# Optimization experiments

Measured on AMD Instinct MI355X. Metric: run time of the kernel, lower is better.

The kernel has to match this reference:

```python
import jax, jax.numpy as jnp
import numpy as np

NUM_HEADS = 16
NUM_KV_HEADS = 4
HEAD_DIM = 128
EPS = 1e-6


def _rotate_half(x):
    x1, x2 = jnp.split(x, 2, axis=-1)
    return jnp.concatenate((-x2, x1), axis=-1)


def _rms_norm(x, w):
    var = jnp.mean(x * x, axis=-1, keepdims=True)
    return x * jax.lax.rsqrt(var + EPS) * w


def setup_inputs() -> dict:
    key = jax.random.key(0)
    ks = jax.random.split(key, 6)
    B, S, H = 2, 2048, 2048
    hidden_states = jax.random.normal(ks[0], (B, S, H), dtype=jnp.float32)
    # real RoPE tables (HF-style: freqs tiled twice along last dim)
    inv_freq = 1.0 / (10000.0 ** (np.arange(0, HEAD_DIM, 2, dtype=np.float32) / HEAD_DIM))
    pos = np.arange(S, dtype=np.float32)
    ang = np.concatenate([pos[:, None] * inv_freq[None, :]] * 2, axis=-1)  # [S, head_dim]
    cos = jnp.broadcast_to(jnp.cos(ang)[None], (B, S, HEAD_DIM)).astype(jnp.float32)
    sin = jnp.broadcast_to(jnp.sin(ang)[None], (B, S, HEAD_DIM)).astype(jnp.float32)
    sc = 0.02
    Wq = jax.random.normal(ks[1], (NUM_HEADS * HEAD_DIM, H), dtype=jnp.float32) * sc
    Wk = jax.random.normal(ks[2], (NUM_KV_HEADS * HEAD_DIM, H), dtype=jnp.float32) * sc
    Wv = jax.random.normal(ks[3], (NUM_KV_HEADS * HEAD_DIM, H), dtype=jnp.float32) * sc
    Wo = jax.random.normal(ks[4], (H, NUM_HEADS * HEAD_DIM), dtype=jnp.float32) * sc
    q_norm_w = jnp.ones((HEAD_DIM,), dtype=jnp.float32)
    k_norm_w = jnp.ones((HEAD_DIM,), dtype=jnp.float32)
    return {"hidden_states": hidden_states, "cos": cos, "sin": sin,
            "Wq": Wq, "Wk": Wk, "Wv": Wv, "Wo": Wo,
            "q_norm_w": q_norm_w, "k_norm_w": k_norm_w}


def reference(hidden_states, cos, sin, Wq, Wk, Wv, Wo, q_norm_w, k_norm_w):
    B, S, H = hidden_states.shape
    groups = NUM_HEADS // NUM_KV_HEADS
    # projections (Linear: x @ W^T), then [B, h, S, d]
    q = (hidden_states @ Wq.T).reshape(B, S, NUM_HEADS, HEAD_DIM).transpose(0, 2, 1, 3)
    k = (hidden_states @ Wk.T).reshape(B, S, NUM_KV_HEADS, HEAD_DIM).transpose(0, 2, 1, 3)
    v = (hidden_states @ Wv.T).reshape(B, S, NUM_KV_HEADS, HEAD_DIM).transpose(0, 2, 1, 3)
    # per-head RMSNorm
    q = _rms_norm(q, q_norm_w)
    k = _rms_norm(k, k_norm_w)
    # RoPE, cos/sin broadcast over heads (unsqueeze_dim=1)
    c = cos[:, None, :, :]
    s = sin[:, None, :, :]
    q = q * c + _rotate_half(q) * s
    k = k * c + _rotate_half(k) * s
    # GQA: expand kv heads
    k = jnp.repeat(k, groups, axis=1)
    v = jnp.repeat(v, groups, axis=1)
    scale = 1.0 / jnp.sqrt(jnp.float32(HEAD_DIM))
    scores = jnp.einsum('bhqd,bhkd->bhqk', q, k) * scale
    attn = jax.nn.softmax(scores, axis=-1)
    out = jnp.einsum('bhqk,bhkd->bhqd', attn, v)
    out = out.transpose(0, 2, 1, 3).reshape(B, S, NUM_HEADS * HEAD_DIM)
    return out @ Wo.T
```

## Files before the change

### kernel.cpp

```cpp
#include <hip/hip_runtime.h>
#include <hip/hip_bf16.h>
#include <stdint.h>

typedef __attribute__((ext_vector_type(8))) short short8;
typedef __attribute__((ext_vector_type(4))) float floatx4;
typedef __attribute__((ext_vector_type(16))) float floatx16;

#define MFMA16(a, b, c) __builtin_amdgcn_mfma_f32_16x16x32_bf16(a, b, c, 0, 0, 0)
#define MFMA32(a, b, c) __builtin_amdgcn_mfma_f32_32x32x16_bf16(a, b, c, 0, 0, 0)

static __device__ __forceinline__ void gload_lds16(const __hip_bfloat16* g, __hip_bfloat16* l) {
  __builtin_amdgcn_global_load_lds(
      (const __attribute__((address_space(1))) void*)g,
      (__attribute__((address_space(3))) void*)l,
      16, 0, 0);
}

__global__ void f2bf(const float* __restrict__ in, __hip_bfloat16* __restrict__ out, int n) {
  const int stride = gridDim.x * blockDim.x * 4;
  for (int i = (blockIdx.x * blockDim.x + threadIdx.x) * 4; i < n; i += stride) {
    const float4 v = *(const float4*)(in + i);
    __hip_bfloat16 t[4] = {__float2bfloat16(v.x), __float2bfloat16(v.y),
                           __float2bfloat16(v.z), __float2bfloat16(v.w)};
    *(short4*)(out + i) = *(const short4*)t;
  }
}

template <typename OUT_T>
__global__ __launch_bounds__(256)
void gemm_bt(const __hip_bfloat16* __restrict__ A, const __hip_bfloat16* __restrict__ Bt,
             OUT_T* __restrict__ C, int M, int N, int K) {
  __shared__ __hip_bfloat16 As[2][128 * 32];
  __shared__ __hip_bfloat16 Bs[2][128 * 32];
  const int tid = threadIdx.x;
  const int wid = tid >> 6, lane = tid & 63;
  const int lg = lane >> 4, lr = lane & 15;
  const int wr = wid >> 1, wc = wid & 1;
  const int m0 = blockIdx.x * 128, n0 = blockIdx.y * 128;
  const int nk = K >> 5;

  floatx4 acc[4][4];
#pragma unroll
  for (int mi = 0; mi < 4; ++mi)
#pragma unroll
    for (int ni = 0; ni < 4; ++ni) acc[mi][ni] = (floatx4)(0.0f);

  auto stage = [&](int buf, int kt) {
    const int k0 = kt << 5;
#pragma unroll
    for (int i = 0; i < 2; ++i) {
      const int e = (i * 256 + tid) * 8;
      const int row = e >> 5, col = e & 31;
      gload_lds16(A + (size_t)(m0 + row) * K + k0 + col, &As[buf][e]);
    }
#pragma unroll
    for (int i = 0; i < 2; ++i) {
      const int e = (i * 256 + tid) * 8;
      const int row = e >> 5, col = e & 31;
      gload_lds16(Bt + (size_t)(n0 + row) * K + k0 + col, &Bs[buf][e]);
    }
  };

  stage(0, 0);
  __syncthreads();

  for (int kt = 0; kt < nk; ++kt) {
    const int cur = kt & 1;
    if (kt + 1 < nk) stage(cur ^ 1, kt + 1);
    short8 af[4], bfr[4];
#pragma unroll
    for (int mi = 0; mi < 4; ++mi)
      af[mi] = *(const short8*)&As[cur][(wr * 64 + mi * 16 + lr) * 32 + lg * 8];
#pragma unroll
    for (int ni = 0; ni < 4; ++ni)
      bfr[ni] = *(const short8*)&Bs[cur][(wc * 64 + ni * 16 + lr) * 32 + lg * 8];
#pragma unroll
    for (int mi = 0; mi < 4; ++mi)
#pragma unroll
      for (int ni = 0; ni < 4; ++ni) acc[mi][ni] = MFMA16(af[mi], bfr[ni], acc[mi][ni]);
    __syncthreads();
  }

#pragma unroll
  for (int mi = 0; mi < 4; ++mi)
#pragma unroll
    for (int ni = 0; ni < 4; ++ni) {
      const int row = m0 + wr * 64 + mi * 16 + lg * 4;
      const int col = n0 + wc * 64 + ni * 16 + lr;
#pragma unroll
      for (int r = 0; r < 4; ++r) {
        C[(size_t)(row + r) * N + col] = (OUT_T)acc[mi][ni][r];
      }
    }
}

__global__ __launch_bounds__(256)
void normrope(const __hip_bfloat16* __restrict__ qkv, const float* __restrict__ cosb,
              const float* __restrict__ sinb, const float* __restrict__ qw,
              const float* __restrict__ kw, __hip_bfloat16* __restrict__ Q,
              __hip_bfloat16* __restrict__ K, __hip_bfloat16* __restrict__ V) {
  const int m = blockIdx.x;
  const int b = m >> 11, s = m & 2047;
  const int wid = threadIdx.x >> 6, lane = threadIdx.x & 63;
  const size_t qkvrow = (size_t)m * 3072;
  const float c1 = cosb[(size_t)m * 128 + lane], s1 = sinb[(size_t)m * 128 + lane];
  const float c2 = cosb[(size_t)m * 128 + lane + 64], s2 = sinb[(size_t)m * 128 + lane + 64];
  for (int h = wid * 6; h < wid * 6 + 6; ++h) {
    const float x1 = __bfloat162float(qkv[qkvrow + h * 128 + lane]);
    const float x2 = __bfloat162float(qkv[qkvrow + h * 128 + lane + 64]);
    if (h < 20) {
      float ss = x1 * x1 + x2 * x2;
      ss += __shfl_xor(ss, 1);  ss += __shfl_xor(ss, 2);  ss += __shfl_xor(ss, 4);
      ss += __shfl_xor(ss, 8);  ss += __shfl_xor(ss, 16); ss += __shfl_xor(ss, 32);
      const float rs = rsqrtf(ss * (1.0f / 128.0f) + 1e-6f);
      const float* w = (h < 16) ? qw : kw;
      const float n1 = x1 * rs * w[lane], n2 = x2 * rs * w[lane + 64];
      const float o1 = n1 * c1 - n2 * s1;
      const float o2 = n2 * c2 + n1 * s2;
      if (h < 16) {
        const size_t base = ((size_t)(b * 16 + h) * 2048 + s) * 128;
        Q[base + lane] = __float2bfloat16(o1);
        Q[base + lane + 64] = __float2bfloat16(o2);
      } else {
        const size_t base = ((size_t)(b * 4 + h - 16) * 2048 + s) * 128;
        K[base + lane] = __float2bfloat16(o1);
        K[base + lane + 64] = __float2bfloat16(o2);
      }
    } else {
      const size_t base = ((size_t)(b * 4 + h - 20) * 2048 + s) * 128;
      V[base + lane] = qkv[qkvrow + h * 128 + lane];
      V[base + lane + 64] = qkv[qkvrow + h * 128 + lane + 64];
    }
  }
}

__global__ __launch_bounds__(256)
void vtrans(const __hip_bfloat16* __restrict__ V, __hip_bfloat16* __restrict__ Vt) {
  __shared__ short L[64 * 65];
  const int tid = threadIdx.x;
  const int s0 = blockIdx.x * 64, d0 = blockIdx.y * 64, bz = blockIdx.z;
  const __hip_bfloat16* src = V + (size_t)bz * 2048 * 128;
#pragma unroll
  for (int i = 0; i < 2; ++i) {
    const int slot = i * 256 + tid;
    const int srow = slot >> 3, c8 = (slot & 7) * 8;
    short8 v = *(const short8*)(src + (size_t)(s0 + srow) * 128 + d0 + c8);
#pragma unroll
    for (int j = 0; j < 8; ++j) L[(c8 + j) * 65 + srow] = v[j];
  }
  __syncthreads();
  __hip_bfloat16* dst = Vt + (size_t)bz * 128 * 2048;
#pragma unroll
  for (int i = 0; i < 2; ++i) {
    const int slot = i * 256 + tid;
    const int drow = slot >> 3, sc8 = (slot & 7) * 8;
    short8 o;
#pragma unroll
    for (int j = 0; j < 8; ++j) {
      const int p = sc8 + j;
      const int pb = p & 31;
      const int phys = (p & ~31) | ((pb & 3) + ((pb >> 2) & 1) * 8 + ((pb >> 3) & 1) * 4 + (pb & 16));
      o[j] = L[drow * 65 + phys];
    }
    *(short8*)(dst + (size_t)(d0 + drow) * 2048 + s0 + sc8) = o;
  }
}

__global__ __launch_bounds__(256, 2)
void fattn(const __hip_bfloat16* __restrict__ Qg, const __hip_bfloat16* __restrict__ Kg,
           const __hip_bfloat16* __restrict__ Vtg, __hip_bfloat16* __restrict__ Og) {
  __shared__ short SMEM[2][17920];

  const int tid = threadIdx.x, wid = tid >> 6, lane = tid & 63;
  const int l31 = lane & 31, hi = lane >> 5;
  const int qt = blockIdx.x, bh = blockIdx.y;
  const int b = bh >> 4, h = bh & 15, hkv = h >> 2;
  const int q0w = qt * 128 + wid * 32;

  const __hip_bfloat16* Qrow = Qg + ((size_t)((b * 16 + h) * 2048 + q0w + l31)) * 128;
  short8 qf2[8];
#pragma unroll
  for (int ks = 0; ks < 8; ++ks) qf2[ks] = *(const short8*)(Qrow + ks * 16 + hi * 8);

  const __hip_bfloat16* Kbase = Kg + (size_t)(b * 4 + hkv) * 2048 * 128;
  const __hip_bfloat16* Vtbase = Vtg + (size_t)(b * 4 + hkv) * 128 * 2048;

  int koff[4], kldsoff[4], voff[4], vldsoff[4];
#pragma unroll
  for (int i = 0; i < 4; ++i) {
    const int idx = i * 256 + tid;
    const int kkv = idx >> 4, kd = (idx & 15) * 8;
    koff[i] = kkv * 128 + kd;
    kldsoff[i] = kkv * 136 + kd;
    const int vd = idx >> 3, vc = (idx & 7) * 8;
    voff[i] = vd * 2048 + vc;
    vldsoff[i] = 8704 + vd * 72 + vc;
  }

  floatx16 oacc[4];
#pragma unroll
  for (int dblk = 0; dblk < 4; ++dblk) oacc[dblk] = (floatx16)(0.0f);
  floatx16 lacc = (floatx16)(0.0f);

  short8 ones;
#pragma unroll
  for (int j = 0; j < 8; ++j) ones[j] = (short)0x3F80;

  const float SC2 = 0.12753102497113446f;
  const float OFF2 = 17.31234049066756f;

  short8 kreg[4], vreg[4];
  auto loadKV = [&](int kt) {
    const __hip_bfloat16* kp = Kbase + (size_t)kt * 64 * 128;
    const __hip_bfloat16* vp = Vtbase + (size_t)kt * 64;
#pragma unroll
    for (int i = 0; i < 4; ++i) kreg[i] = *(const short8*)(kp + koff[i]);
#pragma unroll
    for (int i = 0; i < 4; ++i) vreg[i] = *(const short8*)(vp + voff[i]);
  };

  loadKV(0);
#pragma unroll
  for (int i = 0; i < 4; ++i) *(short8*)&SMEM[0][kldsoff[i]] = kreg[i];
#pragma unroll
  for (int i = 0; i < 4; ++i) *(short8*)&SMEM[0][vldsoff[i]] = vreg[i];
  loadKV(1);
  asm volatile("s_waitcnt lgkmcnt(0)" ::: "memory");
  __builtin_amdgcn_s_barrier();
  __builtin_amdgcn_sched_barrier(0);

  for (int kt = 0; kt < 32; ++kt) {
    const int cur = kt & 1;
    const short* Ksf = SMEM[cur];
    const short* Vtl = SMEM[cur];
    if (kt + 1 < 32) {
      short* nb = SMEM[cur ^ 1];
#pragma unroll
      for (int i = 0; i < 4; ++i) *(short8*)&nb[kldsoff[i]] = kreg[i];
#pragma unroll
      for (int i = 0; i < 4; ++i) *(short8*)&nb[vldsoff[i]] = vreg[i];
      if (kt + 2 < 32) loadKV(kt + 2);
    }

    floatx16 st[2];
    st[0] = (floatx16)(0.0f);
    st[1] = (floatx16)(0.0f);
    __builtin_amdgcn_s_setprio(1);
#pragma unroll
    for (int ks = 0; ks < 8; ++ks) {
      const short8 kf0 = *(const short8*)&Ksf[l31 * 136 + ks * 16 + hi * 8];
      const short8 kf1 = *(const short8*)&Ksf[(32 + l31) * 136 + ks * 16 + hi * 8];
      st[0] = MFMA32(kf0, qf2[ks], st[0]);
      st[1] = MFMA32(kf1, qf2[ks], st[1]);
    }
    __builtin_amdgcn_s_setprio(0);

    int pk[2][8];
#pragma unroll
    for (int kvblk = 0; kvblk < 2; ++kvblk)
#pragma unroll
      for (int m = 0; m < 8; ++m) {
        const float e0 = exp2f(fmaf(st[kvblk][2 * m], SC2, -OFF2));
        const float e1 = exp2f(fmaf(st[kvblk][2 * m + 1], SC2, -OFF2));
        asm("v_cvt_pk_bf16_f32 %0, %1, %2" : "=v"(pk[kvblk][m]) : "v"(e0), "v"(e1));
      }

#pragma unroll
    for (int kvblk = 0; kvblk < 2; ++kvblk) {
#pragma unroll
      for (int s = 0; s < 2; ++s) {
        union { int i[4]; short8 s8; } u;
        u.i[0] = pk[kvblk][4 * s + 0];
        u.i[1] = pk[kvblk][4 * s + 1];
        u.i[2] = pk[kvblk][4 * s + 2];
        u.i[3] = pk[kvblk][4 * s + 3];
        const short8 pB = u.s8;
        __builtin_amdgcn_s_setprio(1);
        lacc = MFMA32(ones, pB, lacc);
#pragma unroll
        for (int dblk = 0; dblk < 4; ++dblk) {
          const short8 vf =
              *(const short8*)&Vtl[8704 + (dblk * 32 + l31) * 72 + kvblk * 32 + s * 16 + hi * 8];
          oacc[dblk] = MFMA32(vf, pB, oacc[dblk]);
        }
        __builtin_amdgcn_s_setprio(0);
      }
    }

    asm volatile("s_waitcnt lgkmcnt(0)" ::: "memory");
    __builtin_amdgcn_s_barrier();
    __builtin_amdgcn_sched_barrier(0);
  }

  const float inv = 1.0f / lacc[0];
  short* tw = &SMEM[0][0] + wid * 4352;
#pragma unroll
  for (int dblk = 0; dblk < 4; ++dblk)
#pragma unroll
    for (int a = 0; a < 4; ++a) {
      __hip_bfloat16 o4[4];
#pragma unroll
      for (int r = 0; r < 4; ++r) o4[r] = __float2bfloat16(oacc[dblk][4 * a + r] * inv);
      *(short4*)&tw[l31 * 136 + dblk * 32 + a * 8 + hi * 4] = *(const short4*)o4;
    }
  __hip_bfloat16* orow =
      Og + ((size_t)(b * 2048 + q0w + (lane >> 1))) * 2048 + h * 128 + (lane & 1) * 64;
  const short* trow = &tw[(lane >> 1) * 136 + (lane & 1) * 64];
#pragma unroll
  for (int c = 0; c < 8; ++c) {
    *(short8*)(orow + c * 8) = *(const short8*)(trow + c * 8);
  }
}

extern "C" void kernel_launch(void* const* d_in, const int* in_sizes, int n_in,
                              void* d_out, int out_size, void* d_ws, size_t ws_size,
                              hipStream_t stream) {
  const float* hidden = (const float*)d_in[0];
  const float* cosb = (const float*)d_in[1];
  const float* sinb = (const float*)d_in[2];
  const float* Wq = (const float*)d_in[3];
  const float* Wk = (const float*)d_in[4];
  const float* Wv = (const float*)d_in[5];
  const float* Wo = (const float*)d_in[6];
  const float* qw = (const float*)d_in[7];
  const float* kw = (const float*)d_in[8];

  char* ws = (char*)d_ws;
  __hip_bfloat16* hidden_bf = (__hip_bfloat16*)ws; ws += (size_t)4096 * 2048 * 2;
  __hip_bfloat16* wqkv = (__hip_bfloat16*)ws;      ws += (size_t)3072 * 2048 * 2;
  __hip_bfloat16* wo_bf = (__hip_bfloat16*)ws;     ws += (size_t)2048 * 2048 * 2;
  __hip_bfloat16* qkv = (__hip_bfloat16*)ws;       ws += (size_t)4096 * 3072 * 2;
  __hip_bfloat16* Qb = (__hip_bfloat16*)ws;        ws += (size_t)2 * 16 * 2048 * 128 * 2;
  __hip_bfloat16* Kb = (__hip_bfloat16*)ws;        ws += (size_t)2 * 4 * 2048 * 128 * 2;
  __hip_bfloat16* Vb = (__hip_bfloat16*)ws;        ws += (size_t)2 * 4 * 2048 * 128 * 2;
  __hip_bfloat16* attn = (__hip_bfloat16*)ws;      ws += (size_t)4096 * 2048 * 2;
  __hip_bfloat16* Vt = wqkv;

  f2bf<<<1024, 256, 0, stream>>>(hidden, hidden_bf, 4096 * 2048);
  f2bf<<<1024, 256, 0, stream>>>(Wq, wqkv, 2048 * 2048);
  f2bf<<<512, 256, 0, stream>>>(Wk, wqkv + (size_t)2048 * 2048, 512 * 2048);
  f2bf<<<512, 256, 0, stream>>>(Wv, wqkv + (size_t)2560 * 2048, 512 * 2048);
  f2bf<<<1024, 256, 0, stream>>>(Wo, wo_bf, 2048 * 2048);

  gemm_bt<__hip_bfloat16><<<dim3(32, 24), 256, 0, stream>>>(hidden_bf, wqkv, qkv, 4096, 3072, 2048);
  normrope<<<4096, 256, 0, stream>>>(qkv, cosb, sinb, qw, kw, Qb, Kb, Vb);
  vtrans<<<dim3(32, 2, 8), 256, 0, stream>>>(Vb, Vt);
  fattn<<<dim3(16, 32), 256, 0, stream>>>(Qb, Kb, Vt, attn);
  gemm_bt<float><<<dim3(32, 16), 256, 0, stream>>>(attn, wo_bf, (float*)d_out, 4096, 2048, 2048);
}
```

Measured before the change: 243.5 us.

## Pre-block K/V tiles and stage them via direct global-to-LDS loads in attention

K and V are re-laid out into contiguous per-tile blocks by new kblock and vtrans2 kernels, with V transposed straight from the qkv buffer so the V copy in normrope goes away. The attention kernel then stages each K/V tile with global_load_lds instead of going through registers and LDS stores. The row sum is now accumulated in VALU from the exponentials instead of an extra MFMA against a ones vector. The intent is to cut register pressure and LDS store traffic in the attention loop, at the cost of an extra kernel pass over K and an unpadded LDS layout that may cause bank conflicts.

```diff
diff --git a/kernel.cpp b/kernel.cpp
--- a/kernel.cpp
+++ b/kernel.cpp
@@ -98,58 +98,68 @@
 void normrope(const __hip_bfloat16* __restrict__ qkv, const float* __restrict__ cosb,
               const float* __restrict__ sinb, const float* __restrict__ qw,
               const float* __restrict__ kw, __hip_bfloat16* __restrict__ Q,
-              __hip_bfloat16* __restrict__ K, __hip_bfloat16* __restrict__ V) {
+              __hip_bfloat16* __restrict__ K) {
   const int m = blockIdx.x;
   const int b = m >> 11, s = m & 2047;
   const int wid = threadIdx.x >> 6, lane = threadIdx.x & 63;
   const size_t qkvrow = (size_t)m * 3072;
   const float c1 = cosb[(size_t)m * 128 + lane], s1 = sinb[(size_t)m * 128 + lane];
   const float c2 = cosb[(size_t)m * 128 + lane + 64], s2 = sinb[(size_t)m * 128 + lane + 64];
-  for (int h = wid * 6; h < wid * 6 + 6; ++h) {
+  for (int h = wid * 5; h < wid * 5 + 5; ++h) {
     const float x1 = __bfloat162float(qkv[qkvrow + h * 128 + lane]);
     const float x2 = __bfloat162float(qkv[qkvrow + h * 128 + lane + 64]);
-    if (h < 20) {
-      float ss = x1 * x1 + x2 * x2;
-      ss += __shfl_xor(ss, 1);  ss += __shfl_xor(ss, 2);  ss += __shfl_xor(ss, 4);
-      ss += __shfl_xor(ss, 8);  ss += __shfl_xor(ss, 16); ss += __shfl_xor(ss, 32);
-      const float rs = rsqrtf(ss * (1.0f / 128.0f) + 1e-6f);
-      const float* w = (h < 16) ? qw : kw;
-      const float n1 = x1 * rs * w[lane], n2 = x2 * rs * w[lane + 64];
-      const float o1 = n1 * c1 - n2 * s1;
-      const float o2 = n2 * c2 + n1 * s2;
-      if (h < 16) {
-        const size_t base = ((size_t)(b * 16 + h) * 2048 + s) * 128;
-        Q[base + lane] = __float2bfloat16(o1);
-        Q[base + lane + 64] = __float2bfloat16(o2);
-      } else {
-        const size_t base = ((size_t)(b * 4 + h - 16) * 2048 + s) * 128;
-        K[base + lane] = __float2bfloat16(o1);
-        K[base + lane + 64] = __float2bfloat16(o2);
-      }
+    float ss = x1 * x1 + x2 * x2;
+    ss += __shfl_xor(ss, 1);  ss += __shfl_xor(ss, 2);  ss += __shfl_xor(ss, 4);
+    ss += __shfl_xor(ss, 8);  ss += __shfl_xor(ss, 16); ss += __shfl_xor(ss, 32);
+    const float rs = rsqrtf(ss * (1.0f / 128.0f) + 1e-6f);
+    const float* w = (h < 16) ? qw : kw;
+    const float n1 = x1 * rs * w[lane], n2 = x2 * rs * w[lane + 64];
+    const float o1 = n1 * c1 - n2 * s1;
+    const float o2 = n2 * c2 + n1 * s2;
+    if (h < 16) {
+      const size_t base = ((size_t)(b * 16 + h) * 2048 + s) * 128;
+      Q[base + lane] = __float2bfloat16(o1);
+      Q[base + lane + 64] = __float2bfloat16(o2);
     } else {
-      const size_t base = ((size_t)(b * 4 + h - 20) * 2048 + s) * 128;
-      V[base + lane] = qkv[qkvrow + h * 128 + lane];
-      V[base + lane + 64] = qkv[qkvrow + h * 128 + lane + 64];
+      const size_t base = ((size_t)(b * 4 + h - 16) * 2048 + s) * 128;
+      K[base + lane] = __float2bfloat16(o1);
+      K[base + lane + 64] = __float2bfloat16(o2);
     }
   }
 }
 
 __global__ __launch_bounds__(256)
-void vtrans(const __hip_bfloat16* __restrict__ V, __hip_bfloat16* __restrict__ Vt) {
+void kblock(const __hip_bfloat16* __restrict__ K, __hip_bfloat16* __restrict__ Kb2) {
+  const int z = blockIdx.y;
+  const int t = blockIdx.x * 4 + (threadIdx.x >> 6);
+  const int kv = threadIdx.x & 63;
+  const short* src = (const short*)K + (size_t)z * 262144 + t * 8192;
+  short* dst = (short*)Kb2 + (size_t)z * 262144 + t * 8192;
+#pragma unroll
+  for (int cd = 0; cd < 16; ++cd) {
+    const short8 v = *(const short8*)&src[kv * 128 + cd * 8];
+    *(short8*)&dst[cd * 512 + kv * 8] = v;
+  }
+}
+
+__global__ __launch_bounds__(256)
+void vtrans2(const __hip_bfloat16* __restrict__ qkv, __hip_bfloat16* __restrict__ Vt2) {
   __shared__ short L[64 * 65];
   const int tid = threadIdx.x;
-  const int s0 = blockIdx.x * 64, d0 = blockIdx.y * 64, bz = blockIdx.z;
-  const __hip_bfloat16* src = V + (size_t)bz * 2048 * 128;
+  const int t = blockIdx.x, d0 = blockIdx.y * 64, z = blockIdx.z;
+  const int b = z >> 2, hkv = z & 3;
+  const int s0 = t * 64;
 #pragma unroll
   for (int i = 0; i < 2; ++i) {
     const int slot = i * 256 + tid;
     const int srow = slot >> 3, c8 = (slot & 7) * 8;
-    short8 v = *(const short8*)(src + (size_t)(s0 + srow) * 128 + d0 + c8);
+    const short8 v = *(const short8*)((const short*)qkv +
+        (size_t)(b * 2048 + s0 + srow) * 3072 + 2560 + hkv * 128 + d0 + c8);
 #pragma unroll
     for (int j = 0; j < 8; ++j) L[(c8 + j) * 65 + srow] = v[j];
   }
   __syncthreads();
-  __hip_bfloat16* dst = Vt + (size_t)bz * 128 * 2048;
+  short* dst = (short*)Vt2 + (size_t)z * 262144 + t * 8192;
 #pragma unroll
   for (int i = 0; i < 2; ++i) {
     const int slot = i * 256 + tid;
@@ -162,19 +172,20 @@
       const int phys = (p & ~31) | ((pb & 3) + ((pb >> 2) & 1) * 8 + ((pb >> 3) & 1) * 4 + (pb & 16));
       o[j] = L[drow * 65 + phys];
     }
-    *(short8*)(dst + (size_t)(d0 + drow) * 2048 + s0 + sc8) = o;
+    *(short8*)&dst[(sc8 >> 3) * 1024 + (d0 + drow) * 8] = o;
   }
 }
 
 __global__ __launch_bounds__(256, 2)
-void fattn(const __hip_bfloat16* __restrict__ Qg, const __hip_bfloat16* __restrict__ Kg,
-           const __hip_bfloat16* __restrict__ Vtg, __hip_bfloat16* __restrict__ Og) {
-  __shared__ short SMEM[2][17920];
+void fattn(const __hip_bfloat16* __restrict__ Qg, const __hip_bfloat16* __restrict__ Kb2,
+           const __hip_bfloat16* __restrict__ Vt2, __hip_bfloat16* __restrict__ Og) {
+  __shared__ short SMEM[2][16384];
 
   const int tid = threadIdx.x, wid = tid >> 6, lane = tid & 63;
   const int l31 = lane & 31, hi = lane >> 5;
   const int qt = blockIdx.x, bh = blockIdx.y;
   const int b = bh >> 4, h = bh & 15, hkv = h >> 2;
+  const int z = b * 4 + hkv;
   const int q0w = qt * 128 + wid * 32;
 
   const __hip_bfloat16* Qrow = Qg + ((size_t)((b * 16 + h) * 2048 + q0w + l31)) * 128;
@@ -182,65 +193,40 @@
 #pragma unroll
   for (int ks = 0; ks < 8; ++ks) qf2[ks] = *(const short8*)(Qrow + ks * 16 + hi * 8);
 
-  const __hip_bfloat16* Kbase = Kg + (size_t)(b * 4 + hkv) * 2048 * 128;
-  const __hip_bfloat16* Vtbase = Vtg + (size_t)(b * 4 + hkv) * 128 * 2048;
-
-  int koff[4], kldsoff[4], voff[4], vldsoff[4];
-#pragma unroll
-  for (int i = 0; i < 4; ++i) {
-    const int idx = i * 256 + tid;
-    const int kkv = idx >> 4, kd = (idx & 15) * 8;
-    koff[i] = kkv * 128 + kd;
-    kldsoff[i] = kkv * 136 + kd;
-    const int vd = idx >> 3, vc = (idx & 7) * 8;
-    voff[i] = vd * 2048 + vc;
-    vldsoff[i] = 8704 + vd * 72 + vc;
-  }
+  const short* Kbase = (const short*)Kb2 + (size_t)z * 262144;
+  const short* Vbase = (const short*)Vt2 + (size_t)z * 262144;
+
+  auto stage = [&](int buf, int t) {
+    const short* ks = Kbase + t * 8192 + wid * 2048 + lane * 8;
+    const short* vs = Vbase + t * 8192 + wid * 2048 + lane * 8;
+    short* kd = &SMEM[buf][wid * 2048];
+    short* vd = &SMEM[buf][8192 + wid * 2048];
+#pragma unroll
+    for (int i = 0; i < 4; ++i)
+      gload_lds16((const __hip_bfloat16*)(ks + i * 512), (__hip_bfloat16*)(kd + i * 512));
+#pragma unroll
+    for (int i = 0; i < 4; ++i)
+      gload_lds16((const __hip_bfloat16*)(vs + i * 512), (__hip_bfloat16*)(vd + i * 512));
+  };
 
   floatx16 oacc[4];
 #pragma unroll
   for (int dblk = 0; dblk < 4; ++dblk) oacc[dblk] = (floatx16)(0.0f);
-  floatx16 lacc = (floatx16)(0.0f);
-
-  short8 ones;
-#pragma unroll
-  for (int j = 0; j < 8; ++j) ones[j] = (short)0x3F80;
+  float la0 = 0.0f, la1 = 0.0f;
 
   const float SC2 = 0.12753102497113446f;
   const float OFF2 = 17.31234049066756f;
 
-  short8 kreg[4], vreg[4];
-  auto loadKV = [&](int kt) {
-    const __hip_bfloat16* kp = Kbase + (size_t)kt * 64 * 128;
-    const __hip_bfloat16* vp = Vtbase + (size_t)kt * 64;
-#pragma unroll
-    for (int i = 0; i < 4; ++i) kreg[i] = *(const short8*)(kp + koff[i]);
-#pragma unroll
-    for (int i = 0; i < 4; ++i) vreg[i] = *(const short8*)(vp + voff[i]);
-  };
-
-  loadKV(0);
-#pragma unroll
-  for (int i = 0; i < 4; ++i) *(short8*)&SMEM[0][kldsoff[i]] = kreg[i];
-#pragma unroll
-  for (int i = 0; i < 4; ++i) *(short8*)&SMEM[0][vldsoff[i]] = vreg[i];
-  loadKV(1);
-  asm volatile("s_waitcnt lgkmcnt(0)" ::: "memory");
+  stage(0, 0);
+  asm volatile("s_waitcnt vmcnt(0)" ::: "memory");
   __builtin_amdgcn_s_barrier();
   __builtin_amdgcn_sched_barrier(0);
 
-  for (int kt = 0; kt < 32; ++kt) {
-    const int cur = kt & 1;
-    const short* Ksf = SMEM[cur];
-    const short* Vtl = SMEM[cur];
-    if (kt + 1 < 32) {
-      short* nb = SMEM[cur ^ 1];
-#pragma unroll
-      for (int i = 0; i < 4; ++i) *(short8*)&nb[kldsoff[i]] = kreg[i];
-#pragma unroll
-      for (int i = 0; i < 4; ++i) *(short8*)&nb[vldsoff[i]] = vreg[i];
-      if (kt + 2 < 32) loadKV(kt + 2);
-    }
+  for (int t = 0; t < 32; ++t) {
+    const int cur = t & 1;
+    const short* Kt = SMEM[cur];
+    const short* Vt = SMEM[cur] + 8192;
+    if (t + 1 < 32) stage(cur ^ 1, t + 1);
 
     floatx16 st[2];
     st[0] = (floatx16)(0.0f);
@@ -248,8 +234,8 @@
     __builtin_amdgcn_s_setprio(1);
 #pragma unroll
     for (int ks = 0; ks < 8; ++ks) {
-      const short8 kf0 = *(const short8*)&Ksf[l31 * 136 + ks * 16 + hi * 8];
-      const short8 kf1 = *(const short8*)&Ksf[(32 + l31) * 136 + ks * 16 + hi * 8];
+      const short8 kf0 = *(const short8*)&Kt[(ks * 2 + hi) * 512 + l31 * 8];
+      const short8 kf1 = *(const short8*)&Kt[(ks * 2 + hi) * 512 + 256 + l31 * 8];
       st[0] = MFMA32(kf0, qf2[ks], st[0]);
       st[1] = MFMA32(kf1, qf2[ks], st[1]);
     }
@@ -262,6 +248,7 @@
       for (int m = 0; m < 8; ++m) {
         const float e0 = exp2f(fmaf(st[kvblk][2 * m], SC2, -OFF2));
         const float e1 = exp2f(fmaf(st[kvblk][2 * m + 1], SC2, -OFF2));
+        if (m & 1) la1 += e0 + e1; else la0 += e0 + e1;
         asm("v_cvt_pk_bf16_f32 %0, %1, %2" : "=v"(pk[kvblk][m]) : "v"(e0), "v"(e1));
       }
 
@@ -275,24 +262,25 @@
         u.i[2] = pk[kvblk][4 * s + 2];
         u.i[3] = pk[kvblk][4 * s + 3];
         const short8 pB = u.s8;
+        const int c = kvblk * 4 + s * 2 + hi;
         __builtin_amdgcn_s_setprio(1);
-        lacc = MFMA32(ones, pB, lacc);
 #pragma unroll
         for (int dblk = 0; dblk < 4; ++dblk) {
-          const short8 vf =
-              *(const short8*)&Vtl[8704 + (dblk * 32 + l31) * 72 + kvblk * 32 + s * 16 + hi * 8];
+          const short8 vf = *(const short8*)&Vt[c * 1024 + dblk * 256 + l31 * 8];
           oacc[dblk] = MFMA32(vf, pB, oacc[dblk]);
         }
         __builtin_amdgcn_s_setprio(0);
       }
     }
 
-    asm volatile("s_waitcnt lgkmcnt(0)" ::: "memory");
+    asm volatile("s_waitcnt vmcnt(0)" ::: "memory");
     __builtin_amdgcn_s_barrier();
     __builtin_amdgcn_sched_barrier(0);
   }
 
-  const float inv = 1.0f / lacc[0];
+  const float l_own = la0 + la1;
+  const float l = l_own + __shfl_xor(l_own, 32);
+  const float inv = 1.0f / l;
   short* tw = &SMEM[0][0] + wid * 4352;
 #pragma unroll
   for (int dblk = 0; dblk < 4; ++dblk)
@@ -332,9 +320,9 @@
   __hip_bfloat16* qkv = (__hip_bfloat16*)ws;       ws += (size_t)4096 * 3072 * 2;
   __hip_bfloat16* Qb = (__hip_bfloat16*)ws;        ws += (size_t)2 * 16 * 2048 * 128 * 2;
   __hip_bfloat16* Kb = (__hip_bfloat16*)ws;        ws += (size_t)2 * 4 * 2048 * 128 * 2;
-  __hip_bfloat16* Vb = (__hip_bfloat16*)ws;        ws += (size_t)2 * 4 * 2048 * 128 * 2;
+  __hip_bfloat16* Kb2 = (__hip_bfloat16*)ws;       ws += (size_t)2 * 4 * 2048 * 128 * 2;
   __hip_bfloat16* attn = (__hip_bfloat16*)ws;      ws += (size_t)4096 * 2048 * 2;
-  __hip_bfloat16* Vt = wqkv;
+  __hip_bfloat16* Vt2 = wqkv;
 
   f2bf<<<1024, 256, 0, stream>>>(hidden, hidden_bf, 4096 * 2048);
   f2bf<<<1024, 256, 0, stream>>>(Wq, wqkv, 2048 * 2048);
@@ -343,8 +331,9 @@
   f2bf<<<1024, 256, 0, stream>>>(Wo, wo_bf, 2048 * 2048);
 
   gemm_bt<__hip_bfloat16><<<dim3(32, 24), 256, 0, stream>>>(hidden_bf, wqkv, qkv, 4096, 3072, 2048);
-  normrope<<<4096, 256, 0, stream>>>(qkv, cosb, sinb, qw, kw, Qb, Kb, Vb);
-  vtrans<<<dim3(32, 2, 8), 256, 0, stream>>>(Vb, Vt);
-  fattn<<<dim3(16, 32), 256, 0, stream>>>(Qb, Kb, Vt, attn);
+  normrope<<<4096, 256, 0, stream>>>(qkv, cosb, sinb, qw, kw, Qb, Kb);
+  kblock<<<dim3(8, 8), 256, 0, stream>>>(Kb, Kb2);
+  vtrans2<<<dim3(32, 2, 8), 256, 0, stream>>>(qkv, Vt2);
+  fattn<<<dim3(16, 32), 256, 0, stream>>>(Qb, Kb2, Vt2, attn);
   gemm_bt<float><<<dim3(32, 16), 256, 0, stream>>>(attn, wo_bf, (float*)d_out, 4096, 2048, 2048);
 }
```

New measurement: 244.0 us. Within noise of the previous version (+0.2%).
